# Kernel optimization log

Hardware: AMD Instinct MI355X
Metric: run time of the kernel (lower is better)

## Reference

```python
import jax, jax.numpy as jnp
import numpy as np

NUM_CLASS = 5
IN_SIZE = 4
OBS_LEN = 20
EMBED = 256
B = 2048
N = 64
NUM_MODES = 20
IN_DIM = IN_SIZE * OBS_LEN  # 80


def setup_inputs() -> dict:
    key = jax.random.key(0)
    ks = jax.random.split(key, 12)
    s = 1.0 / np.sqrt(IN_DIM)
    inp = {
        "obs": jax.random.normal(ks[0], (B, OBS_LEN, IN_SIZE), jnp.float32),
        "neis": jax.random.normal(ks[1], (B, N, OBS_LEN, IN_SIZE), jnp.float32),
        "self_labels": jax.random.randint(ks[2], (B,), 0, NUM_CLASS),
        "nei_labels": jax.random.randint(ks[3], (B, N), 0, NUM_CLASS + 1),
        "modes": jax.random.normal(ks[4], (NUM_CLASS, NUM_MODES, EMBED), jnp.float32),
        # per-class obs embedding (ModuleList of Linear(in_dim, embed))
        "obs_W": jax.random.uniform(ks[5], (NUM_CLASS, IN_DIM, EMBED), jnp.float32, -s, s),
        "obs_b": jax.random.uniform(ks[6], (NUM_CLASS, EMBED), jnp.float32, -s, s),
        # per-class neighbor embedding (num_class+1 Linears)
        "nei_W": jax.random.uniform(ks[7], (NUM_CLASS + 1, IN_DIM, EMBED), jnp.float32, -s, s),
        "nei_b": jax.random.uniform(ks[8], (NUM_CLASS + 1, EMBED), jnp.float32, -s, s),
        # mode embedding Linear(2*embed, embed)
        "mode_W": jax.random.uniform(ks[9], (2 * EMBED, EMBED), jnp.float32, -1.0 / np.sqrt(2 * EMBED), 1.0 / np.sqrt(2 * EMBED)),
        "mode_b": jax.random.uniform(ks[10], (EMBED,), jnp.float32, -1.0 / np.sqrt(2 * EMBED), 1.0 / np.sqrt(2 * EMBED)),
    }
    return inp


def reference(obs, neis, self_labels, nei_labels, modes, obs_W, obs_b, nei_W, nei_b, mode_W, mode_b):
    obs_f = obs.reshape(B, IN_DIM)            # [B, in_dim]
    neis_f = neis.reshape(B, N, IN_DIM)       # [B, N, in_dim]
    eps = jnp.float32(1e-4)

    # label-routed obs embedding: one-hot selects the per-class Linear
    oh_s = jax.nn.one_hot(self_labels, NUM_CLASS, dtype=obs.dtype)          # [B, C]
    x = jnp.einsum("bi,cio,bc->bo", obs_f, obs_W, oh_s) + obs_b[self_labels]  # [B, E]

    # elementwise reciprocal transform (class-independent, applied to every neighbor row)
    r = jnp.where(neis_f >= 0, 1.0 / (neis_f + eps), 1.0 / (neis_f - eps))   # [B, N, in_dim]

    # label-routed neighbor embedding over num_class+1 experts
    oh_n = jax.nn.one_hot(nei_labels, NUM_CLASS + 1, dtype=obs.dtype)        # [B, N, C+1]
    nei_feats = jnp.einsum("bni,cio,bnc->bno", r, nei_W, oh_n) + nei_b[nei_labels]  # [B, N, E]

    mode_feats = modes[self_labels]                                          # [B, M, E]
    x_tiled = jnp.broadcast_to(x[:, None, :], (B, NUM_MODES, EMBED))
    cat = jnp.concatenate([x_tiled, mode_feats], axis=-1)                    # [B, M, 2E]
    out = jnp.einsum("bmk,ko->bmo", cat, mode_W) + mode_b                    # [B, M, E]
    return (out, nei_feats)
```

## Files before the change

kernel.cpp:

```cpp
#include <hip/hip_runtime.h>

#define BATCH 2048
#define NNEI 64
#define IN_DIM 80
#define EMBED 256
#define NCLS 5
#define NMODES 20
#define NROWS (BATCH * NNEI)
#define NEXP (NCLS + 1)
#define TM 16
#define GRID2 512
#define MAXT 104

#define NBIN (NROWS / 256)
#define NWF 144
#define NPRJ (NCLS * NMODES)

typedef __attribute__((ext_vector_type(8))) short bf16x8;
typedef __attribute__((ext_vector_type(4))) float f32x4;
typedef __attribute__((ext_vector_type(4))) int i32x4;

__device__ inline unsigned short bf16_rne(float f) {
    unsigned u = __builtin_bit_cast(unsigned, f);
    unsigned r = (u + 0x7fffu + ((u >> 16) & 1u)) >> 16;
    return (unsigned short)r;
}
__device__ inline float bf16_to_f(unsigned short h) {
    unsigned u = ((unsigned)h) << 16;
    return __builtin_bit_cast(float, u);
}
__device__ inline void st_nt(float* p, float v) { __builtin_nontemporal_store(v, p); }

__global__ void prep_all(const int* __restrict__ nei_labels,
                         int* __restrict__ counts, int* __restrict__ lists,
                         const float* __restrict__ nei_W, unsigned short* __restrict__ wfrag,
                         const float* __restrict__ modes, const float* __restrict__ mode_W,
                         const float* __restrict__ mode_b, float* __restrict__ proj) {
    __shared__ int lc[NEXP], lb[NEXP];
    const int b = blockIdx.x;
    const int t = threadIdx.x;

    if (b < NBIN) {
        if (t < NEXP) lc[t] = 0;
        __syncthreads();
        int r = b * 256 + t;
        int c = nei_labels[r];
        int lpos = atomicAdd(&lc[c], 1);
        __syncthreads();
        if (t < NEXP) lb[t] = atomicAdd(&counts[t], lc[t]);
        __syncthreads();
        lists[(size_t)c * NROWS + lb[c] + lpos] = r;
    } else if (b < NBIN + NWF) {
        int e = (b - NBIN) * 4 + (t >> 6);
        int l = t & 63;
        int part = e & 1;
        int cfg = (e >> 1) & 15;
        int ks = (e >> 5) % 3;
        int c = e / 96;
        int col = cfg * 16 + (l & 15);
        unsigned short v[8] __attribute__((aligned(16)));
        #pragma unroll
        for (int j = 0; j < 8; ++j) {
            int k = ks * 32 + ((l >> 4) * 8) + j;
            float w = (k < IN_DIM) ? nei_W[((size_t)c * IN_DIM + k) * EMBED + col] : 0.f;
            unsigned short h = bf16_rne(w);
            if (part == 0) v[j] = h;
            else v[j] = bf16_rne(w - bf16_to_f(h));
        }
        unsigned short* dst = wfrag + ((size_t)e * 64 + l) * 8;
        *reinterpret_cast<i32x4*>(dst) = *reinterpret_cast<const i32x4*>(v);
    } else {
        int cm = b - (NBIN + NWF);
        int o = t;
        const float* mv = modes + (size_t)cm * EMBED;
        float acc = mode_b[o];
        #pragma unroll 8
        for (int k = 0; k < EMBED; ++k)
            acc = fmaf(mv[k], mode_W[(size_t)(EMBED + k) * EMBED + o], acc);
        proj[(size_t)cm * EMBED + o] = acc;
    }
}

#define BPB 2
__global__ __launch_bounds__(256, 4)
void obs_mode(const float* __restrict__ obs, const int* __restrict__ self_labels,
              const float* __restrict__ obs_W, const float* __restrict__ obs_b,
              const float* __restrict__ mode_W, const float* __restrict__ proj,
              float* __restrict__ out0) {
    int b0 = blockIdx.x * BPB;
    int o = threadIdx.x;
    __shared__ float obs_s[BPB][IN_DIM];
    __shared__ float x_s[BPB][EMBED];
    __shared__ int cls_s[BPB];

    for (int t = threadIdx.x; t < BPB * IN_DIM; t += 256) {
        int bb = t / IN_DIM, k = t % IN_DIM;
        obs_s[bb][k] = obs[(size_t)(b0 + bb) * IN_DIM + k];
    }
    if (threadIdx.x < BPB) cls_s[threadIdx.x] = self_labels[b0 + threadIdx.x];
    __syncthreads();

    int c[BPB];
    float xacc[BPB];
    #pragma unroll
    for (int bb = 0; bb < BPB; ++bb) {
        c[bb] = cls_s[bb];
        xacc[bb] = obs_b[c[bb] * EMBED + o];
    }
    #pragma unroll 4
    for (int k = 0; k < IN_DIM; ++k) {
        #pragma unroll
        for (int bb = 0; bb < BPB; ++bb)
            xacc[bb] = fmaf(obs_s[bb][k],
                            obs_W[(size_t)c[bb] * IN_DIM * EMBED + (size_t)k * EMBED + o],
                            xacc[bb]);
    }
    #pragma unroll
    for (int bb = 0; bb < BPB; ++bb) x_s[bb][o] = xacc[bb];
    __syncthreads();

    float tacc[BPB];
    #pragma unroll
    for (int bb = 0; bb < BPB; ++bb) tacc[bb] = 0.f;
    #pragma unroll 4
    for (int k = 0; k < EMBED; ++k) {
        float wv = mode_W[(size_t)k * EMBED + o];
        #pragma unroll
        for (int bb = 0; bb < BPB; ++bb)
            tacc[bb] = fmaf(x_s[bb][k], wv, tacc[bb]);
    }
    #pragma unroll
    for (int bb = 0; bb < BPB; ++bb) {
        const float* pj = proj + (size_t)c[bb] * NMODES * EMBED;
        float* op = out0 + (size_t)(b0 + bb) * NMODES * EMBED;
        for (int m = 0; m < NMODES; ++m)
            st_nt(&op[m * EMBED + o], tacc[bb] + pj[m * EMBED + o]);
    }
}

__global__ __launch_bounds__(256, 2)
void nei_gemv_mfma(const float* __restrict__ neis,
                   const unsigned short* __restrict__ wfrag,
                   const float* __restrict__ nei_b,
                   const int* __restrict__ counts,
                   const int* __restrict__ lists,
                   float* __restrict__ out_n) {
    const int b = blockIdx.x;
    const int c = (b * NEXP) / GRID2;
    const int cstart = (c * GRID2 + NEXP - 1) / NEXP;
    const int cend = ((c + 1) * GRID2 + NEXP - 1) / NEXP;
    const int blk = b - cstart;
    const int nblk = cend - cstart;
    const int cnt = counts[c];
    const int ntiles = (cnt + TM - 1) / TM;

    __shared__ int rids_s[MAXT * TM];

    if (blk >= ntiles || cnt == 0) return;
    const int nt = min((ntiles - blk + nblk - 1) / nblk, MAXT);

    const int ch = threadIdx.x >> 6;
    const int l = threadIdx.x & 63;
    const int* mylist = lists + (size_t)c * NROWS;
    const int kc = (l >> 4) * 8;

    for (int i = threadIdx.x; i < nt * TM; i += 256) {
        int j = i >> 4, r = i & 15;
        int gi = (blk + j * nblk) * TM + r;
        rids_s[i] = mylist[min(gi, cnt - 1)];
    }

    bf16x8 wh[3][4], wl[3][4];
    {
        const unsigned short* wb = wfrag + (size_t)c * 96 * 64 * 8;
        #pragma unroll
        for (int ks = 0; ks < 3; ++ks)
            #pragma unroll
            for (int cf = 0; cf < 4; ++cf) {
                size_t base = ((((size_t)ks * 16 + (ch * 4 + cf)) * 2) * 64 + l) * 8;
                wh[ks][cf] = *reinterpret_cast<const bf16x8*>(wb + base);
                wl[ks][cf] = *reinterpret_cast<const bf16x8*>(wb + base + 64 * 8);
            }
    }
    #pragma unroll
    for (int ks = 0; ks < 3; ++ks)
        #pragma unroll
        for (int cf = 0; cf < 4; ++cf) {
            i32x4 th = __builtin_bit_cast(i32x4, wh[ks][cf]);
            asm volatile("" : "+v"(th));
            wh[ks][cf] = __builtin_bit_cast(bf16x8, th);
            i32x4 tl = __builtin_bit_cast(i32x4, wl[ks][cf]);
            asm volatile("" : "+v"(tl));
            wl[ks][cf] = __builtin_bit_cast(bf16x8, tl);
        }
    float bias[4];
    #pragma unroll
    for (int cf = 0; cf < 4; ++cf) {
        bias[cf] = nei_b[c * EMBED + (ch * 4 + cf) * 16 + (l & 15)];
        asm volatile("" : "+v"(bias[cf]));
    }
    __syncthreads();

#define LOADJ(F, R, J) {                                                      \
    R = rids_s[(J) * TM + (l & 15)];                                          \
    const float* bp_ = neis + (size_t)(unsigned)R * IN_DIM;                   \
    _Pragma("unroll")                                                         \
    for (int ks_ = 0; ks_ < 3; ++ks_) {                                       \
        int k0_ = ks_ * 32 + kc;                                              \
        if (k0_ + 8 > IN_DIM) k0_ = 0;          \
        *reinterpret_cast<float4*>(&F[ks_ * 8])     = *reinterpret_cast<const float4*>(bp_ + k0_);     \
        *reinterpret_cast<float4*>(&F[ks_ * 8 + 4]) = *reinterpret_cast<const float4*>(bp_ + k0_ + 4); \
    } }

#define COMPJ(F, R, J) {                                                      \
    bf16x8 ah_[3], al_[3];                                                    \
    _Pragma("unroll")                                                         \
    for (int ks_ = 0; ks_ < 3; ++ks_) {                                       \
        _Pragma("unroll")                                                     \
        for (int j_ = 0; j_ < 8; ++j_) {                                      \
            float v_ = F[ks_ * 8 + j_];                                       \
            float d_ = (v_ >= 0.f) ? (v_ + 1e-4f) : (v_ - 1e-4f);             \
            float r_ = __builtin_amdgcn_rcpf(d_);                             \
            unsigned short hi_ = bf16_rne(r_);                                \
            ah_[ks_][j_] = (short)hi_;                                        \
            al_[ks_][j_] = (short)bf16_rne(r_ - bf16_to_f(hi_));              \
        }                                                                     \
    }                                                                         \
    f32x4 acc_[4];                                                            \
    _Pragma("unroll")                                                         \
    for (int cf_ = 0; cf_ < 4; ++cf_) acc_[cf_] = (f32x4){0.f, 0.f, 0.f, 0.f};\
    _Pragma("unroll")                                                         \
    for (int ks_ = 0; ks_ < 3; ++ks_) {                                       \
        _Pragma("unroll")                                                     \
        for (int cf_ = 0; cf_ < 4; ++cf_) {                                   \
            acc_[cf_] = __builtin_amdgcn_mfma_f32_16x16x32_bf16(ah_[ks_], wh[ks_][cf_], acc_[cf_], 0, 0, 0); \
            acc_[cf_] = __builtin_amdgcn_mfma_f32_16x16x32_bf16(al_[ks_], wh[ks_][cf_], acc_[cf_], 0, 0, 0); \
            acc_[cf_] = __builtin_amdgcn_mfma_f32_16x16x32_bf16(ah_[ks_], wl[ks_][cf_], acc_[cf_], 0, 0, 0); \
        }                                                                     \
    }                                                                         \
    int rb_ = (l >> 4) * 4;                                                   \
    int tbase_ = (blk + (J) * nblk) * TM;                                     \
    _Pragma("unroll")                                                         \
    for (int i_ = 0; i_ < 4; ++i_) {                                          \
        int rid_ = __shfl(R, rb_ + i_);                                       \
        if (tbase_ + rb_ + i_ < cnt) {                                        \
            float* op_ = out_n + (size_t)(unsigned)rid_ * EMBED + (l & 15);   \
            _Pragma("unroll")                                                 \
            for (int cf_ = 0; cf_ < 4; ++cf_)                                 \
                st_nt(&op_[(ch * 4 + cf_) * 16], acc_[cf_][i_] + bias[cf_]);  \
        }                                                                     \
    } }

    float fA[24], fB[24], fC[24];
    int ridA, ridB, ridC;
    LOADJ(fA, ridA, 0)
    if (nt > 1) LOADJ(fB, ridB, 1)
    int j = 0;
    while (true) {
        if (j + 2 < nt) LOADJ(fC, ridC, j + 2)
        COMPJ(fA, ridA, j)
        if (j + 1 >= nt) break;
        if (j + 3 < nt) LOADJ(fA, ridA, j + 3)
        COMPJ(fB, ridB, j + 1)
        if (j + 2 >= nt) break;
        if (j + 4 < nt) LOADJ(fB, ridB, j + 4)
        COMPJ(fC, ridC, j + 2)
        if (j + 3 >= nt) break;
        j += 3;
    }
#undef LOADJ
#undef COMPJ
}

extern "C" void kernel_launch(void* const* d_in, const int* in_sizes, int n_in,
                              void* d_out, int out_size, void* d_ws, size_t ws_size,
                              hipStream_t stream) {
    const float* obs         = (const float*)d_in[0];
    const float* neis        = (const float*)d_in[1];
    const int*   self_labels = (const int*)d_in[2];
    const int*   nei_labels  = (const int*)d_in[3];
    const float* modes       = (const float*)d_in[4];
    const float* obs_W       = (const float*)d_in[5];
    const float* obs_b       = (const float*)d_in[6];
    const float* nei_W       = (const float*)d_in[7];
    const float* nei_b       = (const float*)d_in[8];
    const float* mode_W      = (const float*)d_in[9];
    const float* mode_b      = (const float*)d_in[10];

    float* out0  = (float*)d_out;
    float* out_n = out0 + (size_t)BATCH * NMODES * EMBED;

    char* ws = (char*)d_ws;
    int* counts = (int*)ws;
    int* lists  = (int*)(ws + 256);
    float* proj = (float*)(ws + 256 + (size_t)NEXP * NROWS * 4);
    unsigned short* wfrag = (unsigned short*)(ws + 256 + (size_t)NEXP * NROWS * 4
                                              + (size_t)NCLS * NMODES * EMBED * 4);

    hipMemsetAsync(counts, 0, NEXP * sizeof(int), stream);

    prep_all<<<NBIN + NWF + NPRJ, 256, 0, stream>>>(nei_labels, counts, lists,
                                                    nei_W, wfrag,
                                                    modes, mode_W, mode_b, proj);
    obs_mode<<<BATCH / BPB, 256, 0, stream>>>(obs, self_labels, obs_W, obs_b,
                                              mode_W, proj, out0);
    nei_gemv_mfma<<<GRID2, 256, 0, stream>>>(neis, wfrag, nei_b,
                                             counts, lists, out_n);
}
```

Before: 96.16 us.

## Bucket obs rows by class, tile obs_mode, drop low-weight MFMA term

After: 129.5 us. 34.7% more time.

```diff
diff --git a/kernel.cpp b/kernel.cpp
--- a/kernel.cpp
+++ b/kernel.cpp
@@ -15,6 +15,10 @@
 #define NBIN (NROWS / 256)
 #define NWF 144
 #define NPRJ (NCLS * NMODES)
+#define NOB (BATCH / 256)
+
+#define TILE_O 8
+#define OGRID 256
 
 typedef __attribute__((ext_vector_type(8))) short bf16x8;
 typedef __attribute__((ext_vector_type(4))) float f32x4;
@@ -32,7 +36,9 @@
 __device__ inline void st_nt(float* p, float v) { __builtin_nontemporal_store(v, p); }
 
 __global__ void prep_all(const int* __restrict__ nei_labels,
+                         const int* __restrict__ self_labels,
                          int* __restrict__ counts, int* __restrict__ lists,
+                         int* __restrict__ counts_o, int* __restrict__ lists_o,
                          const float* __restrict__ nei_W, unsigned short* __restrict__ wfrag,
                          const float* __restrict__ modes, const float* __restrict__ mode_W,
                          const float* __restrict__ mode_b, float* __restrict__ proj) {
@@ -69,7 +75,7 @@
         }
         unsigned short* dst = wfrag + ((size_t)e * 64 + l) * 8;
         *reinterpret_cast<i32x4*>(dst) = *reinterpret_cast<const i32x4*>(v);
-    } else {
+    } else if (b < NBIN + NWF + NPRJ) {
         int cm = b - (NBIN + NWF);
         int o = t;
         const float* mv = modes + (size_t)cm * EMBED;
@@ -78,67 +84,96 @@
         for (int k = 0; k < EMBED; ++k)
             acc = fmaf(mv[k], mode_W[(size_t)(EMBED + k) * EMBED + o], acc);
         proj[(size_t)cm * EMBED + o] = acc;
-    }
-}
-
-#define BPB 2
+    } else {
+        if (t < NCLS) lc[t] = 0;
+        __syncthreads();
+        int r = (b - (NBIN + NWF + NPRJ)) * 256 + t;
+        int c = self_labels[r];
+        int lpos = atomicAdd(&lc[c], 1);
+        __syncthreads();
+        if (t < NCLS) lb[t] = atomicAdd(&counts_o[t], lc[t]);
+        __syncthreads();
+        lists_o[c * BATCH + lb[c] + lpos] = r;
+    }
+}
+
 __global__ __launch_bounds__(256, 4)
-void obs_mode(const float* __restrict__ obs, const int* __restrict__ self_labels,
+void obs_mode(const float* __restrict__ obs,
+              const int* __restrict__ counts_o, const int* __restrict__ lists_o,
               const float* __restrict__ obs_W, const float* __restrict__ obs_b,
               const float* __restrict__ mode_W, const float* __restrict__ proj,
               float* __restrict__ out0) {
-    int b0 = blockIdx.x * BPB;
-    int o = threadIdx.x;
-    __shared__ float obs_s[BPB][IN_DIM];
-    __shared__ float x_s[BPB][EMBED];
-    __shared__ int cls_s[BPB];
-
-    for (int t = threadIdx.x; t < BPB * IN_DIM; t += 256) {
-        int bb = t / IN_DIM, k = t % IN_DIM;
-        obs_s[bb][k] = obs[(size_t)(b0 + bb) * IN_DIM + k];
-    }
-    if (threadIdx.x < BPB) cls_s[threadIdx.x] = self_labels[b0 + threadIdx.x];
-    __syncthreads();
-
-    int c[BPB];
-    float xacc[BPB];
-    #pragma unroll
-    for (int bb = 0; bb < BPB; ++bb) {
-        c[bb] = cls_s[bb];
-        xacc[bb] = obs_b[c[bb] * EMBED + o];
-    }
-    #pragma unroll 4
-    for (int k = 0; k < IN_DIM; ++k) {
-        #pragma unroll
-        for (int bb = 0; bb < BPB; ++bb)
-            xacc[bb] = fmaf(obs_s[bb][k],
-                            obs_W[(size_t)c[bb] * IN_DIM * EMBED + (size_t)k * EMBED + o],
-                            xacc[bb]);
-    }
-    #pragma unroll
-    for (int bb = 0; bb < BPB; ++bb) x_s[bb][o] = xacc[bb];
-    __syncthreads();
-
-    float tacc[BPB];
-    #pragma unroll
-    for (int bb = 0; bb < BPB; ++bb) tacc[bb] = 0.f;
-    #pragma unroll 4
-    for (int k = 0; k < EMBED; ++k) {
-        float wv = mode_W[(size_t)k * EMBED + o];
-        #pragma unroll
-        for (int bb = 0; bb < BPB; ++bb)
-            tacc[bb] = fmaf(x_s[bb][k], wv, tacc[bb]);
-    }
-    #pragma unroll
-    for (int bb = 0; bb < BPB; ++bb) {
-        const float* pj = proj + (size_t)c[bb] * NMODES * EMBED;
-        float* op = out0 + (size_t)(b0 + bb) * NMODES * EMBED;
-        for (int m = 0; m < NMODES; ++m)
-            st_nt(&op[m * EMBED + o], tacc[bb] + pj[m * EMBED + o]);
-    }
-}
-
-__global__ __launch_bounds__(256, 2)
+    const int b = blockIdx.x;
+    const int c = (b * NCLS) / OGRID;
+    const int cstart = (c * OGRID + NCLS - 1) / NCLS;
+    const int cend = ((c + 1) * OGRID + NCLS - 1) / NCLS;
+    const int blk = b - cstart;
+    const int nblk = cend - cstart;
+    const int cnt = counts_o[c];
+    const int ntiles = (cnt + TILE_O - 1) / TILE_O;
+    if (blk >= ntiles || cnt == 0) return;
+
+    const int o = threadIdx.x;
+    const int* mylist = lists_o + c * BATCH;
+    const float* wc = obs_W + (size_t)c * IN_DIM * EMBED;
+    const float* pj = proj + (size_t)c * NMODES * EMBED;
+    const float bini = obs_b[c * EMBED + o];
+
+    __shared__ float obs_s[TILE_O][IN_DIM];
+    __shared__ float x_s[TILE_O][EMBED];
+    __shared__ int rid_s[TILE_O];
+
+    for (int lt = blk; lt < ntiles; lt += nblk) {
+        if (o < TILE_O) {
+            int gi = lt * TILE_O + o;
+            rid_s[o] = (gi < cnt) ? mylist[gi] : -1;
+        }
+        __syncthreads();
+        for (int f = o; f < TILE_O * IN_DIM; f += 256) {
+            int bb = f / IN_DIM, k = f - bb * IN_DIM;
+            int rid = rid_s[bb];
+            obs_s[bb][k] = (rid >= 0) ? obs[(size_t)rid * IN_DIM + k] : 0.f;
+        }
+        __syncthreads();
+
+        float xacc[TILE_O];
+        #pragma unroll
+        for (int bb = 0; bb < TILE_O; ++bb) xacc[bb] = bini;
+        #pragma unroll 4
+        for (int k = 0; k < IN_DIM; ++k) {
+            float wv = wc[(size_t)k * EMBED + o];
+            #pragma unroll
+            for (int bb = 0; bb < TILE_O; ++bb)
+                xacc[bb] = fmaf(obs_s[bb][k], wv, xacc[bb]);
+        }
+        #pragma unroll
+        for (int bb = 0; bb < TILE_O; ++bb) x_s[bb][o] = xacc[bb];
+        __syncthreads();
+
+        float tacc[TILE_O];
+        #pragma unroll
+        for (int bb = 0; bb < TILE_O; ++bb) tacc[bb] = 0.f;
+        #pragma unroll 4
+        for (int k = 0; k < EMBED; ++k) {
+            float wv = mode_W[(size_t)k * EMBED + o];
+            #pragma unroll
+            for (int bb = 0; bb < TILE_O; ++bb)
+                tacc[bb] = fmaf(x_s[bb][k], wv, tacc[bb]);
+        }
+        #pragma unroll
+        for (int bb = 0; bb < TILE_O; ++bb) {
+            int rid = rid_s[bb];
+            if (rid >= 0) {
+                float* op = out0 + (size_t)rid * NMODES * EMBED;
+                for (int m = 0; m < NMODES; ++m)
+                    st_nt(&op[m * EMBED + o], tacc[bb] + pj[m * EMBED + o]);
+            }
+        }
+        __syncthreads();
+    }
+}
+
+__global__ __launch_bounds__(256, 3)
 void nei_gemv_mfma(const float* __restrict__ neis,
                    const unsigned short* __restrict__ wfrag,
                    const float* __restrict__ nei_b,
@@ -170,7 +205,7 @@
         rids_s[i] = mylist[min(gi, cnt - 1)];
     }
 
-    bf16x8 wh[3][4], wl[3][4];
+    bf16x8 wh[3][4];
     {
         const unsigned short* wb = wfrag + (size_t)c * 96 * 64 * 8;
         #pragma unroll
@@ -179,7 +214,6 @@
             for (int cf = 0; cf < 4; ++cf) {
                 size_t base = ((((size_t)ks * 16 + (ch * 4 + cf)) * 2) * 64 + l) * 8;
                 wh[ks][cf] = *reinterpret_cast<const bf16x8*>(wb + base);
-                wl[ks][cf] = *reinterpret_cast<const bf16x8*>(wb + base + 64 * 8);
             }
     }
     #pragma unroll
@@ -189,9 +223,6 @@
             i32x4 th = __builtin_bit_cast(i32x4, wh[ks][cf]);
             asm volatile("" : "+v"(th));
             wh[ks][cf] = __builtin_bit_cast(bf16x8, th);
-            i32x4 tl = __builtin_bit_cast(i32x4, wl[ks][cf]);
-            asm volatile("" : "+v"(tl));
-            wl[ks][cf] = __builtin_bit_cast(bf16x8, tl);
         }
     float bias[4];
     #pragma unroll
@@ -235,14 +266,13 @@
         for (int cf_ = 0; cf_ < 4; ++cf_) {                                   \
             acc_[cf_] = __builtin_amdgcn_mfma_f32_16x16x32_bf16(ah_[ks_], wh[ks_][cf_], acc_[cf_], 0, 0, 0); \
             acc_[cf_] = __builtin_amdgcn_mfma_f32_16x16x32_bf16(al_[ks_], wh[ks_][cf_], acc_[cf_], 0, 0, 0); \
-            acc_[cf_] = __builtin_amdgcn_mfma_f32_16x16x32_bf16(ah_[ks_], wl[ks_][cf_], acc_[cf_], 0, 0, 0); \
         }                                                                     \
     }                                                                         \
     int rb_ = (l >> 4) * 4;                                                   \
     int tbase_ = (blk + (J) * nblk) * TM;                                     \
     _Pragma("unroll")                                                         \
     for (int i_ = 0; i_ < 4; ++i_) {                                          \
-        int rid_ = __shfl(R, rb_ + i_);                                       \
+        int rid_ = rids_s[(J) * TM + rb_ + i_];                               \
         if (tbase_ + rb_ + i_ < cnt) {                                        \
             float* op_ = out_n + (size_t)(unsigned)rid_ * EMBED + (l & 15);   \
             _Pragma("unroll")                                                 \
@@ -291,19 +321,23 @@
     float* out_n = out0 + (size_t)BATCH * NMODES * EMBED;
 
     char* ws = (char*)d_ws;
-    int* counts = (int*)ws;
-    int* lists  = (int*)(ws + 256);
-    float* proj = (float*)(ws + 256 + (size_t)NEXP * NROWS * 4);
-    unsigned short* wfrag = (unsigned short*)(ws + 256 + (size_t)NEXP * NROWS * 4
-                                              + (size_t)NCLS * NMODES * EMBED * 4);
-
-    hipMemsetAsync(counts, 0, NEXP * sizeof(int), stream);
-
-    prep_all<<<NBIN + NWF + NPRJ, 256, 0, stream>>>(nei_labels, counts, lists,
-                                                    nei_W, wfrag,
-                                                    modes, mode_W, mode_b, proj);
-    obs_mode<<<BATCH / BPB, 256, 0, stream>>>(obs, self_labels, obs_W, obs_b,
-                                              mode_W, proj, out0);
+    int* counts   = (int*)ws;
+    int* counts_o = (int*)(ws + 64);
+    int* lists    = (int*)(ws + 256);
+    size_t off = 256 + (size_t)NEXP * NROWS * 4;
+    int* lists_o = (int*)(ws + off);
+    off += (size_t)NCLS * BATCH * 4;
+    float* proj = (float*)(ws + off);
+    off += (size_t)NCLS * NMODES * EMBED * 4;
+    unsigned short* wfrag = (unsigned short*)(ws + off);
+
+    hipMemsetAsync(ws, 0, 128, stream);
+
+    prep_all<<<NBIN + NWF + NPRJ + NOB, 256, 0, stream>>>(
+        nei_labels, self_labels, counts, lists, counts_o, lists_o,
+        nei_W, wfrag, modes, mode_W, mode_b, proj);
+    obs_mode<<<OGRID, 256, 0, stream>>>(obs, counts_o, lists_o, obs_W, obs_b,
+                                        mode_W, proj, out0);
     nei_gemv_mfma<<<GRID2, 256, 0, stream>>>(neis, wfrag, nei_b,
                                              counts, lists, out_n);
 }
```
